# Optimization experiments

Measured on AMD Instinct MI355X. Metric: run time of the kernel, lower is better.

## Reference

```python
import jax, jax.numpy as jnp
import numpy as np

B, C, H, W, R = 16, 64, 192, 192, 64

def setup_inputs() -> dict:
    key = jax.random.key(0)
    ks = jax.random.split(key, 8)
    return {
        "X":  jax.random.normal(ks[0], (B, C, H, W), dtype=jnp.float32),
        "p":  jnp.ones((R,), dtype=jnp.float32),  # parameter_r init = ones
        "Wc": jax.random.normal(ks[1], (R, C, C), dtype=jnp.float32) * (1.0 / np.sqrt(C)),
        "bc": jax.random.normal(ks[2], (R, C), dtype=jnp.float32) * 0.01,
        "Wh": jax.random.normal(ks[3], (R, H, H), dtype=jnp.float32) * (1.0 / np.sqrt(H)),
        "bh": jax.random.normal(ks[4], (R, H), dtype=jnp.float32) * 0.01,
        "Ww": jax.random.normal(ks[5], (R, W, W), dtype=jnp.float32) * (1.0 / np.sqrt(W)),
        "bw": jax.random.normal(ks[6], (R, W), dtype=jnp.float32) * 0.01,
    }

def reference(X, p, Wc, bc, Wh, bh, Ww, bw):
    # Global average pools (shared across all r iterations; the torch loop
    # recomputes them redundantly every iteration -- same values).
    cp = X.mean(axis=(2, 3))  # [B,C]  pool over H,W
    hp = X.mean(axis=(1, 3))  # [B,H]  pool over C,W (after permute 0,2,1,3)
    wp = X.mean(axis=(1, 2))  # [B,W]  pool over C,H (after permute 0,3,2,1)
    # Per-iteration 1x1 convs on [*,1,1] == batched affine maps, then sigmoid.
    Cw = jax.nn.sigmoid(jnp.einsum('rdc,bc->rbd', Wc, cp) + bc[:, None, :])  # [R,B,C]
    Hw = jax.nn.sigmoid(jnp.einsum('rdh,bh->rbd', Wh, hp) + bh[:, None, :])  # [R,B,H]
    Ww_ = jax.nn.sigmoid(jnp.einsum('rdw,bw->rbd', Ww, wp) + bw[:, None, :])  # [R,B,W]
    # y = sum_r p[r] * C_weight_r x H_weight_r x W_weight_r  (rank-1-per-axis outer)
    y = jnp.einsum('r,rbc,rbh,rbw->bchw', p, Cw, Hw, Ww_)
    return y * X
```

## Files before the change

kernel.cpp:

```cpp
#include <hip/hip_runtime.h>
#include <hip/hip_bf16.h>
#include <math.h>

#define B_  16
#define C_  64
#define H_  192
#define W_  192
#define R_  64
#define HW_ (H_*W_)

#define OFF_CP  0
#define OFF_HP  1024
#define OFF_WP  4096
#define OFF_MC  7168
#define OFF_HWS 72704
#define OFF_WWS 269312

typedef __attribute__((ext_vector_type(8))) short bf16x8;
typedef __attribute__((ext_vector_type(4))) float f32x4;

static __device__ __forceinline__ short f2bf(float f) {
    unsigned u = __float_as_uint(f);
    unsigned r = u + 0x7fffu + ((u >> 16) & 1u);
    return (short)(r >> 16);
}

__global__ __launch_bounds__(256) void zero_kernel(float* p, int n) {
    int i = blockIdx.x * 256 + threadIdx.x;
    if (i < n) p[i] = 0.f;
}

__global__ __launch_bounds__(256) void pool_kernel(const float* __restrict__ X,
                                                   float* __restrict__ cp,
                                                   float* __restrict__ hp,
                                                   float* __restrict__ wp) {
    int b = blockIdx.x >> 6;
    int c = blockIdx.x & 63;
    int tid = threadIdx.x;
    int wv = tid >> 6, lane = tid & 63;
    const float* base = X + (size_t)(b * C_ + c) * HW_ + wv * 48 * W_;

    __shared__ float rowsum[H_];
    __shared__ float colpart[4][W_];
    __shared__ float cpart[3];

    float col0 = 0.f, col1 = 0.f, col2 = 0.f;
    for (int hh = 0; hh < 48; hh += 4) {
        float x[4][3];
        #pragma unroll
        for (int u = 0; u < 4; ++u) {
            #pragma unroll
            for (int k = 0; k < 3; ++k)
                x[u][k] = base[(hh + u) * W_ + k * 64 + lane];
        }
        #pragma unroll
        for (int u = 0; u < 4; ++u) {
            col0 += x[u][0]; col1 += x[u][1]; col2 += x[u][2];
            float s = x[u][0] + x[u][1] + x[u][2];
            s += __shfl_down(s, 32);
            s += __shfl_down(s, 16);
            s += __shfl_down(s, 8);
            s += __shfl_down(s, 4);
            s += __shfl_down(s, 2);
            s += __shfl_down(s, 1);
            if (lane == 0) rowsum[wv * 48 + hh + u] = s;
        }
    }
    colpart[wv][lane]       = col0;
    colpart[wv][lane + 64]  = col1;
    colpart[wv][lane + 128] = col2;
    __syncthreads();

    const float inv_cw = 1.0f / 12288.0f;
    if (tid < 192) {
        float colv = colpart[0][tid] + colpart[1][tid] + colpart[2][tid] + colpart[3][tid];
        atomicAdd(&wp[b * W_ + tid], colv * inv_cw);
        float rv = rowsum[tid];
        atomicAdd(&hp[b * H_ + tid], rv * inv_cw);
        float s = rv;
        s += __shfl_down(s, 32);
        s += __shfl_down(s, 16);
        s += __shfl_down(s, 8);
        s += __shfl_down(s, 4);
        s += __shfl_down(s, 2);
        s += __shfl_down(s, 1);
        if ((tid & 63) == 0) cpart[tid >> 6] = s;
    }
    __syncthreads();
    if (tid == 0) cp[b * C_ + c] = (cpart[0] + cpart[1] + cpart[2]) * (1.0f / (float)HW_);
}

__global__ __launch_bounds__(256) void affine_all_kernel(
        const float* __restrict__ Wc, const float* __restrict__ bc,
        const float* __restrict__ Wh, const float* __restrict__ bh,
        const float* __restrict__ Ww, const float* __restrict__ bw,
        const float* __restrict__ cp, const float* __restrict__ hp,
        const float* __restrict__ wp, const float* __restrict__ p,
        float* __restrict__ Mc, float* __restrict__ Hws, float* __restrict__ Wws) {
    __shared__ float pl[16 * 193];
    int blk = blockIdx.x;
    const float *Wsrc, *bias, *pool, *pmul;
    float* outp;
    int D, K;
    if (blk < 256) {
        Wsrc = Wc; bias = bc; pool = cp; pmul = p; outp = Mc; D = C_; K = C_;
    } else if (blk < 1024) {
        blk -= 256;
        Wsrc = Wh; bias = bh; pool = hp; pmul = nullptr; outp = Hws; D = H_; K = H_;
    } else {
        blk -= 1024;
        Wsrc = Ww; bias = bw; pool = wp; pmul = nullptr; outp = Wws; D = W_; K = W_;
    }

    int tid = threadIdx.x;
    for (int i = tid; i < 16 * K; i += 256) {
        int bb = i / K, kk = i - bb * K;
        pl[bb * (K + 1) + kk] = pool[i];
    }
    __syncthreads();

    int b  = tid & 15;
    int rl = tid >> 4;
    int row = blk * 16 + rl;
    int r = row / D, d = row - r * D;

    const float4* w4 = (const float4*)(Wsrc + (size_t)row * K);
    const float*  pb = &pl[b * (K + 1)];
    float acc = 0.f;
    for (int k4 = 0; k4 < (K >> 2); ++k4) {
        float4 wv = w4[k4];
        int k = k4 << 2;
        acc += wv.x * pb[k] + wv.y * pb[k + 1] + wv.z * pb[k + 2] + wv.w * pb[k + 3];
    }
    acc += bias[row];
    float sgm = 1.0f / (1.0f + expf(-acc));
    if (pmul) sgm *= pmul[r];
    if (D == C_)
        outp[(size_t)b * (C_ * R_) + (size_t)d * R_ + r] = sgm;
    else
        outp[(size_t)b * (D * R_) + (size_t)d * R_ + r] = sgm;
}

__global__ __launch_bounds__(256) void main_kernel(const float* __restrict__ X,
                                                   const float* __restrict__ Mc,
                                                   const float* __restrict__ Hws,
                                                   const float* __restrict__ Wws,
                                                   float* __restrict__ out) {
    int blk = blockIdx.x;
    int b = blk / 576;
    int rem = blk - b * 576;
    int h = rem / 3;
    int w0 = (rem - h * 3) * 64;
    int tid = threadIdx.x;
    int wv = tid >> 6, lane = tid & 63;
    int m = lane & 15, quad = lane >> 4;

    const float* McB = Mc + b * (C_ * R_);
    const float* HvB = Hws + ((size_t)b * H_ + h) * R_;
    const float* WwB = Wws + ((size_t)b * W_ + w0) * R_;

    int wbase = w0 + wv * 16 + quad * 4;
    size_t pixbase = (size_t)h * W_ + wbase;
    float4 xv[4];
    #pragma unroll
    for (int ct = 0; ct < 4; ++ct) {
        int c = ct * 16 + m;
        xv[ct] = *(const float4*)(X + (size_t)(b * C_ + c) * HW_ + pixbase);
    }

    bf16x8 afrag[2];
    #pragma unroll
    for (int ks = 0; ks < 2; ++ks) {
        const float4* wp4 = (const float4*)(WwB + (wv * 16 + m) * R_ + ks * 32 + quad * 8);
        const float4* hp4 = (const float4*)(HvB + ks * 32 + quad * 8);
        float4 w0v = wp4[0], w1v = wp4[1];
        float4 h0v = hp4[0], h1v = hp4[1];
        afrag[ks][0] = f2bf(w0v.x * h0v.x); afrag[ks][1] = f2bf(w0v.y * h0v.y);
        afrag[ks][2] = f2bf(w0v.z * h0v.z); afrag[ks][3] = f2bf(w0v.w * h0v.w);
        afrag[ks][4] = f2bf(w1v.x * h1v.x); afrag[ks][5] = f2bf(w1v.y * h1v.y);
        afrag[ks][6] = f2bf(w1v.z * h1v.z); afrag[ks][7] = f2bf(w1v.w * h1v.w);
    }

    f32x4 acc[4];
    #pragma unroll
    for (int ct = 0; ct < 4; ++ct) acc[ct] = (f32x4){0.f, 0.f, 0.f, 0.f};

    #pragma unroll
    for (int ct = 0; ct < 4; ++ct) {
        #pragma unroll
        for (int ks = 0; ks < 2; ++ks) {
            const float4* bp = (const float4*)(McB + (ct * 16 + m) * R_ + ks * 32 + quad * 8);
            float4 b0 = bp[0], b1 = bp[1];
            bf16x8 bfrag;
            bfrag[0] = f2bf(b0.x); bfrag[1] = f2bf(b0.y);
            bfrag[2] = f2bf(b0.z); bfrag[3] = f2bf(b0.w);
            bfrag[4] = f2bf(b1.x); bfrag[5] = f2bf(b1.y);
            bfrag[6] = f2bf(b1.z); bfrag[7] = f2bf(b1.w);
            acc[ct] = __builtin_amdgcn_mfma_f32_16x16x32_bf16(afrag[ks], bfrag, acc[ct], 0, 0, 0);
        }
    }

    #pragma unroll
    for (int ct = 0; ct < 4; ++ct) {
        int c = ct * 16 + m;
        float4 o;
        o.x = acc[ct][0] * xv[ct].x;
        o.y = acc[ct][1] * xv[ct].y;
        o.z = acc[ct][2] * xv[ct].z;
        o.w = acc[ct][3] * xv[ct].w;
        *(float4*)(out + (size_t)(b * C_ + c) * HW_ + pixbase) = o;
    }
}

extern "C" void kernel_launch(void* const* d_in, const int* in_sizes, int n_in,
                              void* d_out, int out_size, void* d_ws, size_t ws_size,
                              hipStream_t stream) {
    const float* X  = (const float*)d_in[0];
    const float* p  = (const float*)d_in[1];
    const float* Wc = (const float*)d_in[2];
    const float* bc = (const float*)d_in[3];
    const float* Wh = (const float*)d_in[4];
    const float* bh = (const float*)d_in[5];
    const float* Ww = (const float*)d_in[6];
    const float* bw = (const float*)d_in[7];
    float* out = (float*)d_out;
    float* ws  = (float*)d_ws;

    float* cp  = ws + OFF_CP;
    float* hp  = ws + OFF_HP;
    float* wp  = ws + OFF_WP;
    float* Mc  = ws + OFF_MC;
    float* Hws = ws + OFF_HWS;
    float* Wws = ws + OFF_WWS;

    zero_kernel<<<24, 256, 0, stream>>>(hp, 6144);

    pool_kernel<<<B_ * C_, 256, 0, stream>>>(X, cp, hp, wp);

    affine_all_kernel<<<1792, 256, 0, stream>>>(Wc, bc, Wh, bh, Ww, bw,
                                                cp, hp, wp, p, Mc, Hws, Wws);

    main_kernel<<<B_ * 576, 256, 0, stream>>>(X, Mc, Hws, Wws, out);
}
```

Measured before the change: 396.2 us.

## Process 12 rows per block in main kernel with hoisted Mc fragments and prefetch

The main kernel now covers 12 image rows per block instead of one. The bf16 Mc fragments and the W-axis weights are converted and loaded once and reused across those rows. The next row of X is prefetched into a double buffer, and outputs use nontemporal stores. The pool kernel switches to float4 row loads with a shorter shuffle reduction, and the affine kernel uses fast exp and unrolling. The grid shrinks to 768 blocks, which lowers parallelism and adds register pressure in exchange for less redundant fragment work.

```diff
diff --git a/kernel.cpp b/kernel.cpp
--- a/kernel.cpp
+++ b/kernel.cpp
@@ -1,5 +1,4 @@
 #include <hip/hip_runtime.h>
-#include <hip/hip_bf16.h>
 #include <math.h>
 
 #define B_  16
@@ -8,6 +7,7 @@
 #define W_  192
 #define R_  64
 #define HW_ (H_*W_)
+#define HCH 12
 
 #define OFF_CP  0
 #define OFF_HP  1024
@@ -38,42 +38,48 @@
     int c = blockIdx.x & 63;
     int tid = threadIdx.x;
     int wv = tid >> 6, lane = tid & 63;
-    const float* base = X + (size_t)(b * C_ + c) * HW_ + wv * 48 * W_;
+    int sub = lane >> 4;
+    int li  = lane & 15;
+    const float* base = X + (size_t)(b * C_ + c) * HW_ + (size_t)(wv * 48) * W_;
 
     __shared__ float rowsum[H_];
-    __shared__ float colpart[4][W_];
+    __shared__ f32x4 colpart4[4][48];
     __shared__ float cpart[3];
 
-    float col0 = 0.f, col1 = 0.f, col2 = 0.f;
+    f32x4 cacc0 = {0.f,0.f,0.f,0.f}, cacc1 = {0.f,0.f,0.f,0.f}, cacc2 = {0.f,0.f,0.f,0.f};
+
+    #pragma unroll 2
     for (int hh = 0; hh < 48; hh += 4) {
-        float x[4][3];
-        #pragma unroll
-        for (int u = 0; u < 4; ++u) {
-            #pragma unroll
-            for (int k = 0; k < 3; ++k)
-                x[u][k] = base[(hh + u) * W_ + k * 64 + lane];
-        }
-        #pragma unroll
-        for (int u = 0; u < 4; ++u) {
-            col0 += x[u][0]; col1 += x[u][1]; col2 += x[u][2];
-            float s = x[u][0] + x[u][1] + x[u][2];
-            s += __shfl_down(s, 32);
-            s += __shfl_down(s, 16);
-            s += __shfl_down(s, 8);
-            s += __shfl_down(s, 4);
-            s += __shfl_down(s, 2);
-            s += __shfl_down(s, 1);
-            if (lane == 0) rowsum[wv * 48 + hh + u] = s;
-        }
-    }
-    colpart[wv][lane]       = col0;
-    colpart[wv][lane + 64]  = col1;
-    colpart[wv][lane + 128] = col2;
+        const float* rp = base + (size_t)(hh + sub) * W_;
+        f32x4 x0 = *(const f32x4*)(rp + 4 * li);
+        f32x4 x1 = *(const f32x4*)(rp + 4 * (li + 16));
+        f32x4 x2 = *(const f32x4*)(rp + 4 * (li + 32));
+        cacc0 += x0; cacc1 += x1; cacc2 += x2;
+        float s = (x0[0]+x0[1]+x0[2]+x0[3]) + (x1[0]+x1[1]+x1[2]+x1[3])
+                + (x2[0]+x2[1]+x2[2]+x2[3]);
+        s += __shfl_down(s, 8);
+        s += __shfl_down(s, 4);
+        s += __shfl_down(s, 2);
+        s += __shfl_down(s, 1);
+        if (li == 0) rowsum[wv * 48 + hh + sub] = s;
+    }
+    #pragma unroll
+    for (int comp = 0; comp < 4; ++comp) {
+        float t0 = cacc0[comp]; t0 += __shfl_down(t0, 16); t0 += __shfl_down(t0, 32); cacc0[comp] = t0;
+        float t1 = cacc1[comp]; t1 += __shfl_down(t1, 16); t1 += __shfl_down(t1, 32); cacc1[comp] = t1;
+        float t2 = cacc2[comp]; t2 += __shfl_down(t2, 16); t2 += __shfl_down(t2, 32); cacc2[comp] = t2;
+    }
+    if (lane < 16) {
+        colpart4[wv][li]      = cacc0;
+        colpart4[wv][li + 16] = cacc1;
+        colpart4[wv][li + 32] = cacc2;
+    }
     __syncthreads();
 
     const float inv_cw = 1.0f / 12288.0f;
     if (tid < 192) {
-        float colv = colpart[0][tid] + colpart[1][tid] + colpart[2][tid] + colpart[3][tid];
+        const float* cpf = (const float*)colpart4;
+        float colv = cpf[tid] + cpf[192 + tid] + cpf[384 + tid] + cpf[576 + tid];
         atomicAdd(&wp[b * W_ + tid], colv * inv_cw);
         float rv = rowsum[tid];
         atomicAdd(&hp[b * H_ + tid], rv * inv_cw);
@@ -127,18 +133,16 @@
     const float4* w4 = (const float4*)(Wsrc + (size_t)row * K);
     const float*  pb = &pl[b * (K + 1)];
     float acc = 0.f;
+    #pragma unroll 8
     for (int k4 = 0; k4 < (K >> 2); ++k4) {
         float4 wv = w4[k4];
         int k = k4 << 2;
         acc += wv.x * pb[k] + wv.y * pb[k + 1] + wv.z * pb[k + 2] + wv.w * pb[k + 3];
     }
     acc += bias[row];
-    float sgm = 1.0f / (1.0f + expf(-acc));
+    float sgm = 1.0f / (1.0f + __expf(-acc));
     if (pmul) sgm *= pmul[r];
-    if (D == C_)
-        outp[(size_t)b * (C_ * R_) + (size_t)d * R_ + r] = sgm;
-    else
-        outp[(size_t)b * (D * R_) + (size_t)d * R_ + r] = sgm;
+    outp[(size_t)b * (D * R_) + (size_t)d * R_ + r] = sgm;
 }
 
 __global__ __launch_bounds__(256) void main_kernel(const float* __restrict__ X,
@@ -147,68 +151,105 @@
                                                    const float* __restrict__ Wws,
                                                    float* __restrict__ out) {
     int blk = blockIdx.x;
-    int b = blk / 576;
-    int rem = blk - b * 576;
-    int h = rem / 3;
-    int w0 = (rem - h * 3) * 64;
+    int b = blk / 48;
+    int rem = blk - b * 48;
+    int hc = rem / 3;
+    int w0 = (rem - hc * 3) * 64;
+    int h0 = hc * HCH;
     int tid = threadIdx.x;
     int wv = tid >> 6, lane = tid & 63;
     int m = lane & 15, quad = lane >> 4;
 
     const float* McB = Mc + b * (C_ * R_);
-    const float* HvB = Hws + ((size_t)b * H_ + h) * R_;
+    const float* HvB = Hws + (size_t)b * H_ * R_;
     const float* WwB = Wws + ((size_t)b * W_ + w0) * R_;
 
+    bf16x8 bfrag[4][2];
+    #pragma unroll
+    for (int ct = 0; ct < 4; ++ct) {
+        #pragma unroll
+        for (int ks = 0; ks < 2; ++ks) {
+            const float4* bp = (const float4*)(McB + (size_t)(ct * 16 + m) * R_ + ks * 32 + quad * 8);
+            float4 b0 = bp[0], b1 = bp[1];
+            bfrag[ct][ks][0] = f2bf(b0.x); bfrag[ct][ks][1] = f2bf(b0.y);
+            bfrag[ct][ks][2] = f2bf(b0.z); bfrag[ct][ks][3] = f2bf(b0.w);
+            bfrag[ct][ks][4] = f2bf(b1.x); bfrag[ct][ks][5] = f2bf(b1.y);
+            bfrag[ct][ks][6] = f2bf(b1.z); bfrag[ct][ks][7] = f2bf(b1.w);
+        }
+    }
+
+    float4 wwf[2][2];
+    #pragma unroll
+    for (int ks = 0; ks < 2; ++ks) {
+        const float4* wp4 = (const float4*)(WwB + (size_t)(wv * 16 + m) * R_ + ks * 32 + quad * 8);
+        wwf[ks][0] = wp4[0]; wwf[ks][1] = wp4[1];
+    }
+
     int wbase = w0 + wv * 16 + quad * 4;
-    size_t pixbase = (size_t)h * W_ + wbase;
-    float4 xv[4];
-    #pragma unroll
-    for (int ct = 0; ct < 4; ++ct) {
-        int c = ct * 16 + m;
-        xv[ct] = *(const float4*)(X + (size_t)(b * C_ + c) * HW_ + pixbase);
-    }
-
-    bf16x8 afrag[2];
-    #pragma unroll
-    for (int ks = 0; ks < 2; ++ks) {
-        const float4* wp4 = (const float4*)(WwB + (wv * 16 + m) * R_ + ks * 32 + quad * 8);
-        const float4* hp4 = (const float4*)(HvB + ks * 32 + quad * 8);
-        float4 w0v = wp4[0], w1v = wp4[1];
-        float4 h0v = hp4[0], h1v = hp4[1];
-        afrag[ks][0] = f2bf(w0v.x * h0v.x); afrag[ks][1] = f2bf(w0v.y * h0v.y);
-        afrag[ks][2] = f2bf(w0v.z * h0v.z); afrag[ks][3] = f2bf(w0v.w * h0v.w);
-        afrag[ks][4] = f2bf(w1v.x * h1v.x); afrag[ks][5] = f2bf(w1v.y * h1v.y);
-        afrag[ks][6] = f2bf(w1v.z * h1v.z); afrag[ks][7] = f2bf(w1v.w * h1v.w);
-    }
-
-    f32x4 acc[4];
-    #pragma unroll
-    for (int ct = 0; ct < 4; ++ct) acc[ct] = (f32x4){0.f, 0.f, 0.f, 0.f};
-
-    #pragma unroll
-    for (int ct = 0; ct < 4; ++ct) {
+    const float* Xb = X   + (size_t)b * C_ * HW_;
+    float*       Ob = out + (size_t)b * C_ * HW_;
+
+    float4 xv[2][4];
+    {
+        size_t pix0 = (size_t)h0 * W_ + wbase;
+        #pragma unroll
+        for (int ct = 0; ct < 4; ++ct)
+            xv[0][ct] = *(const float4*)(Xb + (size_t)(ct * 16 + m) * HW_ + pix0);
+    }
+
+    #pragma unroll
+    for (int hi = 0; hi < HCH; ++hi) {
+        const int cur = hi & 1;
+        const int nxt = cur ^ 1;
+        int h = h0 + hi;
+
+        float4 hvv[4];
+        const float* Hp = HvB + (size_t)h * R_;
         #pragma unroll
         for (int ks = 0; ks < 2; ++ks) {
-            const float4* bp = (const float4*)(McB + (ct * 16 + m) * R_ + ks * 32 + quad * 8);
-            float4 b0 = bp[0], b1 = bp[1];
-            bf16x8 bfrag;
-            bfrag[0] = f2bf(b0.x); bfrag[1] = f2bf(b0.y);
-            bfrag[2] = f2bf(b0.z); bfrag[3] = f2bf(b0.w);
-            bfrag[4] = f2bf(b1.x); bfrag[5] = f2bf(b1.y);
-            bfrag[6] = f2bf(b1.z); bfrag[7] = f2bf(b1.w);
-            acc[ct] = __builtin_amdgcn_mfma_f32_16x16x32_bf16(afrag[ks], bfrag, acc[ct], 0, 0, 0);
-        }
-    }
-
-    #pragma unroll
-    for (int ct = 0; ct < 4; ++ct) {
-        int c = ct * 16 + m;
-        float4 o;
-        o.x = acc[ct][0] * xv[ct].x;
-        o.y = acc[ct][1] * xv[ct].y;
-        o.z = acc[ct][2] * xv[ct].z;
-        o.w = acc[ct][3] * xv[ct].w;
-        *(float4*)(out + (size_t)(b * C_ + c) * HW_ + pixbase) = o;
+            const float4* hp4 = (const float4*)(Hp + ks * 32 + quad * 8);
+            hvv[2 * ks]     = hp4[0];
+            hvv[2 * ks + 1] = hp4[1];
+        }
+
+        if (hi + 1 < HCH) {
+            size_t pixn = (size_t)(h + 1) * W_ + wbase;
+            #pragma unroll
+            for (int ct = 0; ct < 4; ++ct)
+                xv[nxt][ct] = *(const float4*)(Xb + (size_t)(ct * 16 + m) * HW_ + pixn);
+        }
+
+        bf16x8 afrag[2];
+        #pragma unroll
+        for (int ks = 0; ks < 2; ++ks) {
+            afrag[ks][0] = f2bf(wwf[ks][0].x * hvv[2 * ks].x);
+            afrag[ks][1] = f2bf(wwf[ks][0].y * hvv[2 * ks].y);
+            afrag[ks][2] = f2bf(wwf[ks][0].z * hvv[2 * ks].z);
+            afrag[ks][3] = f2bf(wwf[ks][0].w * hvv[2 * ks].w);
+            afrag[ks][4] = f2bf(wwf[ks][1].x * hvv[2 * ks + 1].x);
+            afrag[ks][5] = f2bf(wwf[ks][1].y * hvv[2 * ks + 1].y);
+            afrag[ks][6] = f2bf(wwf[ks][1].z * hvv[2 * ks + 1].z);
+            afrag[ks][7] = f2bf(wwf[ks][1].w * hvv[2 * ks + 1].w);
+        }
+
+        f32x4 acc[4];
+        #pragma unroll
+        for (int ct = 0; ct < 4; ++ct) {
+            acc[ct] = (f32x4){0.f, 0.f, 0.f, 0.f};
+            acc[ct] = __builtin_amdgcn_mfma_f32_16x16x32_bf16(afrag[0], bfrag[ct][0], acc[ct], 0, 0, 0);
+            acc[ct] = __builtin_amdgcn_mfma_f32_16x16x32_bf16(afrag[1], bfrag[ct][1], acc[ct], 0, 0, 0);
+        }
+
+        size_t pix = (size_t)h * W_ + wbase;
+        #pragma unroll
+        for (int ct = 0; ct < 4; ++ct) {
+            f32x4 o;
+            o[0] = acc[ct][0] * xv[cur][ct].x;
+            o[1] = acc[ct][1] * xv[cur][ct].y;
+            o[2] = acc[ct][2] * xv[cur][ct].z;
+            o[3] = acc[ct][3] * xv[cur][ct].w;
+            __builtin_nontemporal_store(o, (f32x4*)(Ob + (size_t)(ct * 16 + m) * HW_ + pix));
+        }
     }
 }
 
@@ -240,5 +281,5 @@
     affine_all_kernel<<<1792, 256, 0, stream>>>(Wc, bc, Wh, bh, Ww, bw,
                                                 cp, hp, wp, p, Mc, Hws, Wws);
 
-    main_kernel<<<B_ * 576, 256, 0, stream>>>(X, Mc, Hws, Wws, out);
-}
+    main_kernel<<<768, 256, 0, stream>>>(X, Mc, Hws, Wws, out);
+}
```

After: 333.8 us. 1.19x faster.
